# Performance work log

Measured on AMD Instinct MI355X. Metric: run time of the kernel, lower is better.

Reference implementation:

```python
import jax, jax.numpy as jnp
import numpy as np

HEADS, POINTS = 8, 4
EPS = 1e-5
BS, C, H, W = 2, 256, 200, 200


def _layernorm(x, g, b):
    m = x.mean(-1, keepdims=True)
    v = ((x - m) ** 2).mean(-1, keepdims=True)
    return (x - m) / jnp.sqrt(v + EPS) * g + b


def _sine_pos(bs, Hh, Ww, num_feats, temperature=10000.0):
    # mmdet SinePositionalEncoding with all-zeros mask: cumsum of ones -> 1..H / 1..W
    y = jnp.arange(1, Hh + 1, dtype=jnp.float32)
    x = jnp.arange(1, Ww + 1, dtype=jnp.float32)
    dim_t = jnp.arange(num_feats, dtype=jnp.float32)
    dim_t = temperature ** (2.0 * jnp.floor(dim_t / 2.0) / num_feats)

    def interleave(p):  # p: [N, num_feats] -> [sin(p0),cos(p1),sin(p2),...]
        return jnp.stack((jnp.sin(p[:, 0::2]), jnp.cos(p[:, 1::2])), axis=-1).reshape(p.shape[0], -1)

    pos_x = interleave(x[:, None] / dim_t)  # [W, nf]
    pos_y = interleave(y[:, None] / dim_t)  # [H, nf]
    pos = jnp.concatenate([
        jnp.broadcast_to(pos_y[:, None, :], (Hh, Ww, num_feats)),
        jnp.broadcast_to(pos_x[None, :, :], (Hh, Ww, num_feats)),
    ], axis=-1)  # [H, W, 2*nf] (channel order matches cat((pos_y,pos_x),dim=1) after flatten/permute)
    return jnp.broadcast_to(pos.reshape(1, Hh * Ww, 2 * num_feats), (bs, Hh * Ww, 2 * num_feats))


def _bilinear_sample(v, x, y):
    # v: [bs, heads, H, W, hd]; x, y: [bs, heads, N] pixel coords (align_corners=False, zero padding)
    bs, nh, Hh, Ww, hd = v.shape
    vf = v.reshape(bs, nh, Hh * Ww, hd)
    x0 = jnp.floor(x)
    y0 = jnp.floor(y)
    wx = x - x0
    wy = y - y0

    def gather(xi, yi):
        valid = (xi >= 0) & (xi < Ww) & (yi >= 0) & (yi < Hh)
        xc = jnp.clip(xi, 0, Ww - 1).astype(jnp.int32)
        yc = jnp.clip(yi, 0, Hh - 1).astype(jnp.int32)
        idx = yc * Ww + xc
        g = jnp.take_along_axis(vf, idx[..., None], axis=2)  # [bs, nh, N, hd]
        return g * valid[..., None].astype(v.dtype)

    out = gather(x0, y0) * ((1 - wx) * (1 - wy))[..., None]
    out = out + gather(x0 + 1, y0) * (wx * (1 - wy))[..., None]
    out = out + gather(x0, y0 + 1) * ((1 - wx) * wy)[..., None]
    out = out + gather(x0 + 1, y0 + 1) * (wx * wy)[..., None]
    return out


def _dfa_layer(out, ref, pos, Hh, Ww, p):
    bs, Lq, Cc = out.shape
    hd = Cc // HEADS
    q = out + pos
    value = out @ p['vp_w'].T + p['vp_b']  # [bs, Lq, C]
    off = (q @ p['off_w'].T + p['off_b']).reshape(bs, Lq, HEADS, POINTS, 2)
    aw = jax.nn.softmax((q @ p['aw_w'].T + p['aw_b']).reshape(bs, Lq, HEADS, POINTS), axis=-1)
    norm = jnp.array([Ww, Hh], dtype=out.dtype)
    loc = ref[None, :, None, None, :] + off / norm  # [bs, Lq, heads, P, 2] normalized [0,1]
    x = loc[..., 0] * Ww - 0.5
    y = loc[..., 1] * Hh - 0.5
    v = value.reshape(bs, Lq, HEADS, hd).transpose(0, 2, 1, 3).reshape(bs, HEADS, Hh, Ww, hd)
    xt = x.transpose(0, 2, 1, 3).reshape(bs, HEADS, Lq * POINTS)
    yt = y.transpose(0, 2, 1, 3).reshape(bs, HEADS, Lq * POINTS)
    samp = _bilinear_sample(v, xt, yt).reshape(bs, HEADS, Lq, POINTS, hd)
    attn = jnp.einsum('bhqpd,bqhp->bqhd', samp, aw).reshape(bs, Lq, Cc)
    attn = attn @ p['op_w'].T + p['op_b']
    out = _layernorm(out + attn, p['ln1_g'], p['ln1_b'])
    ffn = jax.nn.relu(out @ p['l1_w'].T + p['l1_b']) @ p['l2_w'].T + p['l2_b']
    return _layernorm(out + ffn, p['ln2_g'], p['ln2_b'])


def setup_inputs() -> dict:
    key = jax.random.key(0)
    ks = jax.random.split(key, 20)
    s = 0.02
    L = 3
    return {
        'bev_feat': jax.random.normal(ks[0], (BS, C, H, W), jnp.float32),
        'proj_q_w': jax.random.normal(ks[1], (C, C), jnp.float32) * s,
        'proj_q_b': jax.random.normal(ks[2], (C,), jnp.float32) * s,
        'off_w': jax.random.normal(ks[3], (L, HEADS * POINTS * 2, C), jnp.float32) * s,
        'off_b': jax.random.normal(ks[4], (L, HEADS * POINTS * 2), jnp.float32) * s,
        'aw_w': jax.random.normal(ks[5], (L, HEADS * POINTS, C), jnp.float32) * s,
        'aw_b': jax.random.normal(ks[6], (L, HEADS * POINTS), jnp.float32) * s,
        'vp_w': jax.random.normal(ks[7], (L, C, C), jnp.float32) * s,
        'vp_b': jax.random.normal(ks[8], (L, C), jnp.float32) * s,
        'op_w': jax.random.normal(ks[9], (L, C, C), jnp.float32) * s,
        'op_b': jax.random.normal(ks[10], (L, C), jnp.float32) * s,
        'ln1_g': jnp.ones((L, C), jnp.float32),
        'ln1_b': jnp.zeros((L, C), jnp.float32),
        'l1_w': jax.random.normal(ks[11], (L, C, C), jnp.float32) * s,
        'l1_b': jax.random.normal(ks[12], (L, C), jnp.float32) * s,
        'l2_w': jax.random.normal(ks[13], (L, C, C), jnp.float32) * s,
        'l2_b': jax.random.normal(ks[14], (L, C), jnp.float32) * s,
        'ln2_g': jnp.ones((L, C), jnp.float32),
        'ln2_b': jnp.zeros((L, C), jnp.float32),
    }


def reference(bev_feat, proj_q_w, proj_q_b, off_w, off_b, aw_w, aw_b, vp_w, vp_b,
              op_w, op_b, ln1_g, ln1_b, l1_w, l1_b, l2_w, l2_b, ln2_g, ln2_b):
    bs, Cc, Hh, Ww = bev_feat.shape
    x = bev_feat.reshape(bs, Cc, Hh * Ww).transpose(0, 2, 1)  # [bs, HW, C]
    out = x @ proj_q_w.T + proj_q_b
    # reference points: pixel centers normalized to [0,1]
    ry, rx = jnp.meshgrid(jnp.linspace(0.5, Hh - 0.5, Hh) / Hh,
                          jnp.linspace(0.5, Ww - 0.5, Ww) / Ww, indexing='ij')
    ref = jnp.stack([rx.reshape(-1), ry.reshape(-1)], axis=-1).astype(bev_feat.dtype)  # [HW, 2]
    pos = _sine_pos(bs, Hh, Ww, Cc // 2).astype(bev_feat.dtype)
    n_layers = off_w.shape[0]
    for i in range(n_layers):
        p = dict(off_w=off_w[i], off_b=off_b[i], aw_w=aw_w[i], aw_b=aw_b[i],
                 vp_w=vp_w[i], vp_b=vp_b[i], op_w=op_w[i], op_b=op_b[i],
                 ln1_g=ln1_g[i], ln1_b=ln1_b[i], l1_w=l1_w[i], l1_b=l1_b[i],
                 l2_w=l2_w[i], l2_b=l2_b[i], ln2_g=ln2_g[i], ln2_b=ln2_b[i])
        out = _dfa_layer(out, ref, pos, Hh, Ww, p)
    return out.transpose(0, 2, 1).reshape(bs, Cc, Hh, Ww)
```

## Files before the change

### kernel.cpp

```cpp
#include <hip/hip_runtime.h>
#include <math.h>

#define HEADS 8
#define POINTS 4
#define BSZ 2
#define CDIM 256
#define HH 200
#define WW 200
#define LQ (HH * WW)
#define MTOT (BSZ * LQ)
#define NLAYERS 3

typedef __attribute__((ext_vector_type(8))) short shortx8;
typedef __attribute__((ext_vector_type(4))) float floatx4;

__device__ __forceinline__ ushort f2b(float f) {
    union { float f; unsigned u; } v; v.f = f;
    unsigned r = v.u + 0x7fffu + ((v.u >> 16) & 1u);
    return (ushort)(r >> 16);
}
__device__ __forceinline__ float b2f(ushort b) {
    union { unsigned u; float f; } v; v.u = ((unsigned)b) << 16;
    return v.f;
}
__device__ __forceinline__ float bitsf(unsigned u) {
    union { unsigned u; float f; } v; v.u = u;
    return v.f;
}
__device__ __forceinline__ uint packbf(float lo, float hi) {
    return (uint)f2b(lo) | ((uint)f2b(hi) << 16);
}

__global__ __launch_bounds__(256)
void cvt_kernel(const float* __restrict__ in, ushort* __restrict__ out)
{
    const int i = (blockIdx.x * 256 + threadIdx.x) * 4;
    const float4 v = *(const float4*)(in + i);
    ushort4 o;
    o.x = f2b(v.x); o.y = f2b(v.y); o.z = f2b(v.z); o.w = f2b(v.w);
    *(ushort4*)(out + i) = o;
}

__global__ __launch_bounds__(256)
void build_offaw(const float* __restrict__ offw, const float* __restrict__ offb,
                 const float* __restrict__ aww, const float* __restrict__ awb,
                 ushort* __restrict__ wout, float* __restrict__ bout)
{
    const int blk = blockIdx.x;
    const int i = blk >> 7;
    const int r = blk & 127;
    const int c = threadIdx.x;
    float v = 0.f;
    if (r < 64)      v = offw[((size_t)i * 64 + r) * CDIM + c];
    else if (r < 96) v = aww[((size_t)i * 32 + (r - 64)) * CDIM + c];
    wout[((size_t)i * 128 + r) * CDIM + c] = f2b(v);
    if (c == 0) {
        float bb = 0.f;
        if (r < 64)      bb = offb[i * 64 + r];
        else if (r < 96) bb = awb[i * 32 + (r - 64)];
        bout[i * 128 + r] = bb;
    }
}

__global__ __launch_bounds__(256)
void pos_kernel(ushort* __restrict__ pos)
{
    const int idx = blockIdx.x * 256 + threadIdx.x;
    const int c = idx & 255;
    const int l = idx >> 8;
    const int cc = c & 127;
    const float coord = (c < 128) ? (float)(l / WW + 1) : (float)(l % WW + 1);
    const float expo = (float)(2 * (cc >> 1)) * (1.0f / 128.0f);
    const float t = powf(10000.0f, expo);
    const float ph = coord / t;
    pos[idx] = f2b((cc & 1) ? cosf(ph) : sinf(ph));
}

__global__ __launch_bounds__(256)
void bevT_kernel(const float* __restrict__ in, ushort* __restrict__ out)
{
    __shared__ float tile[32][33];
    const int b = blockIdx.z;
    const int l0 = blockIdx.x * 32;
    const int c0 = blockIdx.y * 32;
    const float* ib = in + (size_t)b * CDIM * LQ;
    ushort* ob = out + (size_t)b * LQ * CDIM;
    #pragma unroll
    for (int j = 0; j < 32; j += 8)
        tile[threadIdx.y + j][threadIdx.x] =
            ib[(size_t)(c0 + threadIdx.y + j) * LQ + l0 + threadIdx.x];
    __syncthreads();
    #pragma unroll
    for (int j = 0; j < 32; j += 8)
        ob[(size_t)(l0 + threadIdx.y + j) * CDIM + c0 + threadIdx.x] =
            f2b(tile[threadIdx.x][threadIdx.y + j]);
}

#define LSTR 40

template<bool RELU, bool F32OUT, bool BF16OUT, bool QOUT>
__global__ __launch_bounds__(256)
void mfma_gemm(const ushort* __restrict__ A, const ushort* __restrict__ B,
               const float* __restrict__ bias,
               float* __restrict__ Cf, ushort* __restrict__ Cb,
               ushort* __restrict__ Cq, const ushort* __restrict__ posb,
               int N, int K)
{
    __shared__ ushort As[128 * LSTR];
    __shared__ ushort Bs[128 * LSTR];
    const int tid = threadIdx.x;
    const int lane = tid & 63;
    const int wave = tid >> 6;
    const int wr = (wave >> 1) * 64;
    const int wc = (wave & 1) * 64;
    const int rowBase = blockIdx.y * 128;
    const int colBase = blockIdx.x * 128;

    floatx4 acc[4][4];
    #pragma unroll
    for (int i = 0; i < 4; i++)
        #pragma unroll
        for (int j = 0; j < 4; j++) {
            floatx4 z = {0.f, 0.f, 0.f, 0.f};
            acc[i][j] = z;
        }

    const int strow = tid >> 2;
    const int stcol = (tid & 3) * 8;
    const int kq = (lane >> 4) * 8;
    const int lr = lane & 15;

    for (int k0 = 0; k0 < K; k0 += 32) {
        #pragma unroll
        for (int j = 0; j < 2; j++) {
            const int r = j * 64 + strow;
            const uint4 av = *(const uint4*)(A + (size_t)(rowBase + r) * K + k0 + stcol);
            const uint4 bv = *(const uint4*)(B + (size_t)(colBase + r) * K + k0 + stcol);
            *(uint4*)(As + r * LSTR + stcol) = av;
            *(uint4*)(Bs + r * LSTR + stcol) = bv;
        }
        __syncthreads();
        shortx8 af[4], bfr[4];
        #pragma unroll
        for (int t = 0; t < 4; t++) {
            af[t]  = *(const shortx8*)(As + (wr + t * 16 + lr) * LSTR + kq);
            bfr[t] = *(const shortx8*)(Bs + (wc + t * 16 + lr) * LSTR + kq);
        }
        #pragma unroll
        for (int mt = 0; mt < 4; mt++)
            #pragma unroll
            for (int nt = 0; nt < 4; nt++)
                acc[mt][nt] = __builtin_amdgcn_mfma_f32_16x16x32_bf16(
                    af[mt], bfr[nt], acc[mt][nt], 0, 0, 0);
        __syncthreads();
    }

    const int colB = colBase + wc + lr;
    const int rowB = rowBase + wr + (lane >> 4) * 4;
    #pragma unroll
    for (int mt = 0; mt < 4; mt++) {
        #pragma unroll
        for (int r = 0; r < 4; r++) {
            const int m = rowB + mt * 16 + r;
            const int pr = (m >= LQ) ? m - LQ : m;
            #pragma unroll
            for (int nt = 0; nt < 4; nt++) {
                const int n = colB + nt * 16;
                float v = acc[mt][nt][r] + bias[n];
                if (RELU) v = fmaxf(v, 0.f);
                if (F32OUT) Cf[(size_t)m * N + n] = v;
                if (BF16OUT) Cb[(size_t)m * N + n] = f2b(v);
                if (QOUT) {
                    const float pv = b2f(posb[(size_t)pr * CDIM + n]);
                    Cq[(size_t)m * N + n] = f2b(v + pv);
                }
            }
        }
    }
}

template<bool RELU, bool LN, bool F32OUT, bool BF16OUT, bool QOUT, bool PERMW>
__global__ __launch_bounds__(256)
void gemm_fused(const ushort* __restrict__ A, const ushort* __restrict__ B,
                const float* __restrict__ bias,
                float* __restrict__ resid, ushort* __restrict__ Cb,
                ushort* __restrict__ Cq, const ushort* __restrict__ posb,
                const float* __restrict__ g, const float* __restrict__ beta)
{
    __shared__ ushort As[64 * LSTR];
    __shared__ ushort Bs[256 * LSTR];
    __shared__ float2 red[64][4];

    const int tid = threadIdx.x;
    const int lane = tid & 63;
    const int wave = tid >> 6;
    const int lr = lane & 15;
    const int hi = lane >> 4;
    const int rowBase = blockIdx.x * 64;
    const int wc = wave * 64;

    floatx4 acc[4][4];
    #pragma unroll
    for (int i = 0; i < 4; i++)
        #pragma unroll
        for (int j = 0; j < 4; j++) {
            floatx4 z = {0.f, 0.f, 0.f, 0.f};
            acc[i][j] = z;
        }

    const int strow = tid >> 2;
    const int stcol = (tid & 3) * 8;
    const int kq = hi * 8;

    const ushort* ag = A + (size_t)(rowBase + strow) * CDIM + stcol;
    const ushort* bg = B + (size_t)strow * CDIM + stcol;

    for (int k0 = 0; k0 < CDIM; k0 += 32) {
        const uint4 av  = *(const uint4*)(ag + k0);
        const uint4 bv0 = *(const uint4*)(bg + k0);
        const uint4 bv1 = *(const uint4*)(bg + k0 + 64 * CDIM);
        const uint4 bv2 = *(const uint4*)(bg + k0 + 128 * CDIM);
        const uint4 bv3 = *(const uint4*)(bg + k0 + 192 * CDIM);
        *(uint4*)(As + strow * LSTR + stcol) = av;
        *(uint4*)(Bs + strow * LSTR + stcol) = bv0;
        *(uint4*)(Bs + (strow + 64) * LSTR + stcol) = bv1;
        *(uint4*)(Bs + (strow + 128) * LSTR + stcol) = bv2;
        *(uint4*)(Bs + (strow + 192) * LSTR + stcol) = bv3;
        __syncthreads();
        shortx8 af[4], bfr[4];
        #pragma unroll
        for (int t = 0; t < 4; t++) {
            af[t]  = *(const shortx8*)(As + (t * 16 + lr) * LSTR + kq);
            bfr[t] = *(const shortx8*)(Bs + (wc + t * 16 + lr) * LSTR + kq);
        }
        #pragma unroll
        for (int mt = 0; mt < 4; mt++)
            #pragma unroll
            for (int nt = 0; nt < 4; nt++)
                acc[mt][nt] = __builtin_amdgcn_mfma_f32_16x16x32_bf16(
                    af[mt], bfr[nt], acc[mt][nt], 0, 0, 0);
        __syncthreads();
    }

    float bcol[4];
    #pragma unroll
    for (int nt = 0; nt < 4; nt++) bcol[nt] = bias[wc + nt * 16 + lr];

    float* pbase = resid + (size_t)blockIdx.x * (64 * CDIM) + wave * 4096 + lane * 64;

    if (LN) {
        #pragma unroll
        for (int mt = 0; mt < 4; mt++) {
            float4 rv[4];
            #pragma unroll
            for (int r = 0; r < 4; r++)
                rv[r] = *(const float4*)(pbase + mt * 16 + r * 4);
            #pragma unroll
            for (int r = 0; r < 4; r++) {
                const int mrel = mt * 16 + hi * 4 + r;
                float s = 0.f, sq = 0.f;
                #pragma unroll
                for (int nt = 0; nt < 4; nt++) {
                    float x = acc[mt][nt][r] + bcol[nt] + (&rv[r].x)[nt];
                    acc[mt][nt][r] = x;
                    s += x; sq += x * x;
                }
                #pragma unroll
                for (int o = 8; o >= 1; o >>= 1) {
                    s  += __shfl_xor(s, o, 64);
                    sq += __shfl_xor(sq, o, 64);
                }
                if (lr == 0) { float2 t2; t2.x = s; t2.y = sq; red[mrel][wave] = t2; }
            }
        }
        __syncthreads();
        float gcol[4], btcol[4];
        #pragma unroll
        for (int nt = 0; nt < 4; nt++) {
            gcol[nt]  = g[wc + nt * 16 + lr];
            btcol[nt] = beta[wc + nt * 16 + lr];
        }
        #pragma unroll
        for (int mt = 0; mt < 4; mt++) {
            #pragma unroll
            for (int r = 0; r < 4; r++) {
                const int mrel = mt * 16 + hi * 4 + r;
                const int m = rowBase + mrel;
                const float2 t0 = red[mrel][0], t1 = red[mrel][1];
                const float2 t2 = red[mrel][2], t3 = red[mrel][3];
                const float S  = (t0.x + t1.x) + (t2.x + t3.x);
                const float SQ = (t0.y + t1.y) + (t2.y + t3.y);
                const float mean = S * (1.0f / CDIM);
                const float var = SQ * (1.0f / CDIM) - mean * mean;
                const float rstd = rsqrtf(var + 1e-5f);
                const int pr = (m >= LQ) ? m - LQ : m;
                float4 wv;
                #pragma unroll
                for (int nt = 0; nt < 4; nt++) {
                    const int col = wc + nt * 16 + lr;
                    const float y = (acc[mt][nt][r] - mean) * rstd * gcol[nt] + btcol[nt];
                    if (PERMW) (&wv.x)[nt] = y;
                    else       resid[(size_t)m * CDIM + col] = y;
                    if (BF16OUT) Cb[(size_t)m * CDIM + col] = f2b(y);
                    if (QOUT) Cq[(size_t)m * CDIM + col] =
                        f2b(y + b2f(posb[(size_t)pr * CDIM + col]));
                }
                if (PERMW) *(float4*)(pbase + mt * 16 + r * 4) = wv;
            }
        }
    } else {
        #pragma unroll
        for (int mt = 0; mt < 4; mt++) {
            #pragma unroll
            for (int r = 0; r < 4; r++) {
                const int m = rowBase + mt * 16 + hi * 4 + r;
                const int pr = (m >= LQ) ? m - LQ : m;
                float4 wv;
                #pragma unroll
                for (int nt = 0; nt < 4; nt++) {
                    const int col = wc + nt * 16 + lr;
                    float y = acc[mt][nt][r] + bcol[nt];
                    if (RELU) y = fmaxf(y, 0.f);
                    if (F32OUT) {
                        if (PERMW) (&wv.x)[nt] = y;
                        else       resid[(size_t)m * CDIM + col] = y;
                    }
                    if (BF16OUT) Cb[(size_t)m * CDIM + col] = f2b(y);
                    if (QOUT) Cq[(size_t)m * CDIM + col] =
                        f2b(y + b2f(posb[(size_t)pr * CDIM + col]));
                }
                if (F32OUT && PERMW) *(float4*)(pbase + mt * 16 + r * 4) = wv;
            }
        }
    }
}

__global__ __launch_bounds__(256)
void sample_kernel(const ushort* __restrict__ val,
                   const float* __restrict__ offaw,
                   ushort* __restrict__ attn)
{
    const int tid = threadIdx.x;
    const int m = blockIdx.x * 8 + (tid >> 5);
    const int lane = tid & 31;
    const int head = lane >> 2;
    const int c = head * 32 + (lane & 3) * 8;
    const int b = (m >= LQ) ? 1 : 0;
    const int l = m - (b ? LQ : 0);

    const float* row = offaw + (size_t)m * 128;
    const float4 lg  = *(const float4*)(row + 64 + head * 4);
    const float4 o01 = *(const float4*)(row + head * 8);
    const float4 o23 = *(const float4*)(row + head * 8 + 4);

    const float mx = fmaxf(fmaxf(lg.x, lg.y), fmaxf(lg.z, lg.w));
    const float e0 = expf(lg.x - mx), e1 = expf(lg.y - mx);
    const float e2 = expf(lg.z - mx), e3 = expf(lg.w - mx);
    const float inv = 1.0f / (e0 + e1 + e2 + e3);
    const float awv[4] = {e0 * inv, e1 * inv, e2 * inv, e3 * inv};

    const float lx = (float)(l % WW);
    const float ly = (float)(l / WW);
    const float px[4] = {lx + o01.x, lx + o01.z, lx + o23.x, lx + o23.z};
    const float py[4] = {ly + o01.y, ly + o01.w, ly + o23.y, ly + o23.w};

    const ushort* vb = val + (size_t)b * LQ * CDIM;
    uint4 cv[16];
    float cw[16];
    #pragma unroll
    for (int p = 0; p < POINTS; p++) {
        const float x = px[p], y = py[p];
        const float xf = floorf(x), yf = floorf(y);
        const int x0 = (int)xf, y0 = (int)yf;
        const float wx = x - xf, wy = y - yf;
        const int x0c = min(max(x0, 0), WW - 1);
        const int x1c = min(max(x0 + 1, 0), WW - 1);
        const int y0c = min(max(y0, 0), HH - 1);
        const int y1c = min(max(y0 + 1, 0), HH - 1);
        const float vx0 = (x0 >= 0 && x0 < WW) ? 1.f : 0.f;
        const float vx1 = (x0 + 1 >= 0 && x0 + 1 < WW) ? 1.f : 0.f;
        const float vy0 = (y0 >= 0 && y0 < HH) ? 1.f : 0.f;
        const float vy1 = (y0 + 1 >= 0 && y0 + 1 < HH) ? 1.f : 0.f;
        const float a = awv[p];
        cw[p * 4 + 0] = a * (1.f - wx) * (1.f - wy) * vx0 * vy0;
        cw[p * 4 + 1] = a * wx * (1.f - wy) * vx1 * vy0;
        cw[p * 4 + 2] = a * (1.f - wx) * wy * vx0 * vy1;
        cw[p * 4 + 3] = a * wx * wy * vx1 * vy1;
        const int r0 = y0c * WW, r1 = y1c * WW;
        cv[p * 4 + 0] = *(const uint4*)(vb + (((unsigned)(r0 + x0c)) << 8) + c);
        cv[p * 4 + 1] = *(const uint4*)(vb + (((unsigned)(r0 + x1c)) << 8) + c);
        cv[p * 4 + 2] = *(const uint4*)(vb + (((unsigned)(r1 + x0c)) << 8) + c);
        cv[p * 4 + 3] = *(const uint4*)(vb + (((unsigned)(r1 + x1c)) << 8) + c);
    }
    float a0 = 0.f, a1 = 0.f, a2 = 0.f, a3 = 0.f;
    float a4 = 0.f, a5 = 0.f, a6 = 0.f, a7 = 0.f;
    #pragma unroll
    for (int i = 0; i < 16; i++) {
        const float wgt = cw[i];
        a0 = fmaf(wgt, bitsf(cv[i].x << 16), a0);
        a1 = fmaf(wgt, bitsf(cv[i].x & 0xffff0000u), a1);
        a2 = fmaf(wgt, bitsf(cv[i].y << 16), a2);
        a3 = fmaf(wgt, bitsf(cv[i].y & 0xffff0000u), a3);
        a4 = fmaf(wgt, bitsf(cv[i].z << 16), a4);
        a5 = fmaf(wgt, bitsf(cv[i].z & 0xffff0000u), a5);
        a6 = fmaf(wgt, bitsf(cv[i].w << 16), a6);
        a7 = fmaf(wgt, bitsf(cv[i].w & 0xffff0000u), a7);
    }
    uint4 o;
    o.x = packbf(a0, a1); o.y = packbf(a2, a3);
    o.z = packbf(a4, a5); o.w = packbf(a6, a7);
    *(uint4*)(attn + (size_t)m * CDIM + c) = o;
}

__global__ __launch_bounds__(256)
void transpose_out(const float* __restrict__ in, float* __restrict__ outp)
{
    __shared__ float tile[32][33];
    const int b = blockIdx.z;
    const int l0 = blockIdx.x * 32;
    const int c0 = blockIdx.y * 32;
    const float* ib = in + (size_t)b * LQ * CDIM;
    float* ob = outp + (size_t)b * CDIM * LQ;
    #pragma unroll
    for (int j = 0; j < 32; j += 8)
        tile[threadIdx.y + j][threadIdx.x] =
            ib[(size_t)(l0 + threadIdx.y + j) * CDIM + c0 + threadIdx.x];
    __syncthreads();
    #pragma unroll
    for (int j = 0; j < 32; j += 8)
        ob[(size_t)(c0 + threadIdx.y + j) * LQ + l0 + threadIdx.x] =
            tile[threadIdx.x][threadIdx.y + j];
}

extern "C" void kernel_launch(void* const* d_in, const int* in_sizes, int n_in,
                              void* d_out, int out_size, void* d_ws, size_t ws_size,
                              hipStream_t stream)
{
    const float* bev      = (const float*)d_in[0];
    const float* proj_q_w = (const float*)d_in[1];
    const float* proj_q_b = (const float*)d_in[2];
    const float* off_w    = (const float*)d_in[3];
    const float* off_b    = (const float*)d_in[4];
    const float* aw_w     = (const float*)d_in[5];
    const float* aw_b     = (const float*)d_in[6];
    const float* vp_w     = (const float*)d_in[7];
    const float* vp_b     = (const float*)d_in[8];
    const float* op_w     = (const float*)d_in[9];
    const float* op_b     = (const float*)d_in[10];
    const float* ln1_g    = (const float*)d_in[11];
    const float* ln1_b    = (const float*)d_in[12];
    const float* l1_w     = (const float*)d_in[13];
    const float* l1_b     = (const float*)d_in[14];
    const float* l2_w     = (const float*)d_in[15];
    const float* l2_b     = (const float*)d_in[16];
    const float* ln2_g    = (const float*)d_in[17];
    const float* ln2_b    = (const float*)d_in[18];
    float* outp = (float*)d_out;

    char* w = (char*)d_ws;
    float*  out_f   = (float*)(w);
    float*  offaw_f = (float*)(w + 81920000);
    ushort* out_b   = (ushort*)(w + 163840000);
    ushort* q_b     = (ushort*)(w + 204800000);
    ushort* val_b   = (ushort*)(w + 245760000);
    ushort* pos_b   = (ushort*)(w + 286720000);
    ushort* w_b     = (ushort*)(w + 307200000);
    ushort* wproj = w_b;
    ushort* wvp   = w_b + 65536;
    ushort* wop   = w_b + 65536 + 196608;
    ushort* wl1   = w_b + 65536 + 2 * 196608;
    ushort* wl2   = w_b + 65536 + 3 * 196608;
    ushort* wofa  = w_b + 65536 + 4 * 196608;
    float*  bofa  = (float*)(w + 307200000 + 2 * (65536 + 4 * 196608 + 98304));

    const dim3 blk(256);

    cvt_kernel<<<dim3(65536 / 1024), blk, 0, stream>>>(proj_q_w, wproj);
    cvt_kernel<<<dim3(196608 / 1024), blk, 0, stream>>>(vp_w, wvp);
    cvt_kernel<<<dim3(196608 / 1024), blk, 0, stream>>>(op_w, wop);
    cvt_kernel<<<dim3(196608 / 1024), blk, 0, stream>>>(l1_w, wl1);
    cvt_kernel<<<dim3(196608 / 1024), blk, 0, stream>>>(l2_w, wl2);
    build_offaw<<<dim3(3 * 128), blk, 0, stream>>>(off_w, off_b, aw_w, aw_b, wofa, bofa);
    pos_kernel<<<dim3((LQ * CDIM) / 256), blk, 0, stream>>>(pos_b);
    bevT_kernel<<<dim3(LQ / 32, CDIM / 32, BSZ), dim3(32, 8), 0, stream>>>(bev, val_b);

    const dim3 gF(MTOT / 64);
    const dim3 g128(1, MTOT / 128);

    gemm_fused<false, false, true, true, true, true><<<gF, blk, 0, stream>>>(
        val_b, wproj, proj_q_b, out_f, out_b, q_b, pos_b, nullptr, nullptr);

    for (int i = 0; i < NLAYERS; i++) {
        gemm_fused<false, false, false, true, false, false><<<gF, blk, 0, stream>>>(
            out_b, wvp + (size_t)i * 65536, vp_b + (size_t)i * CDIM,
            nullptr, val_b, nullptr, nullptr, nullptr, nullptr);
        mfma_gemm<false, true, false, false><<<g128, blk, 0, stream>>>(
            q_b, wofa + (size_t)i * 32768, bofa + (size_t)i * 128,
            offaw_f, nullptr, nullptr, nullptr, 128, CDIM);
        sample_kernel<<<dim3(MTOT / 8), blk, 0, stream>>>(val_b, offaw_f, q_b);
        gemm_fused<false, true, false, true, false, true><<<gF, blk, 0, stream>>>(
            q_b, wop + (size_t)i * 65536, op_b + (size_t)i * CDIM,
            out_f, out_b, nullptr, pos_b,
            ln1_g + (size_t)i * CDIM, ln1_b + (size_t)i * CDIM);
        gemm_fused<true, false, false, true, false, false><<<gF, blk, 0, stream>>>(
            out_b, wl1 + (size_t)i * 65536, l1_b + (size_t)i * CDIM,
            nullptr, val_b, nullptr, nullptr, nullptr, nullptr);
        if (i < NLAYERS - 1) {
            gemm_fused<false, true, false, true, true, true><<<gF, blk, 0, stream>>>(
                val_b, wl2 + (size_t)i * 65536, l2_b + (size_t)i * CDIM,
                out_f, out_b, q_b, pos_b,
                ln2_g + (size_t)i * CDIM, ln2_b + (size_t)i * CDIM);
        } else {
            gemm_fused<false, true, false, false, false, false><<<gF, blk, 0, stream>>>(
                val_b, wl2 + (size_t)i * 65536, l2_b + (size_t)i * CDIM,
                out_f, nullptr, nullptr, pos_b,
                ln2_g + (size_t)i * CDIM, ln2_b + (size_t)i * CDIM);
        }
    }

    transpose_out<<<dim3(LQ / 32, CDIM / 32, BSZ), dim3(32, 8), 0, stream>>>(out_f, outp);
}
```

Before: 1.124 ms.

## Permute channel layout so fused GEMM epilogues write vectorized row stores

Introduces a fixed channel permutation within 64-column groups and applies it consistently to weights (vp, l1, l2, off/aw), positional encodings and the final transpose. With it, each lane's four output columns become contiguous, so GEMM epilogues emit float4/ushort4 stores for the residual, bf16 and query outputs instead of scattered scalar stores. The old per-lane 'PERMW' scratch layout for the fp32 residual is replaced by normal row-major addressing, and the LayerNorm reduction buffer now reuses the As shared memory. The risk is correctness: every producer and consumer of the permuted layout must agree, including the sampling kernel and the un-permute in the output transpose.

```diff
diff --git a/kernel.cpp b/kernel.cpp
--- a/kernel.cpp
+++ b/kernel.cpp
@@ -31,6 +31,13 @@
     return (uint)f2b(lo) | ((uint)f2b(hi) << 16);
 }
 
+__device__ __forceinline__ int permc(int c) {
+    return (c & ~63) | (((c & 15) << 2) | ((c & 63) >> 4));
+}
+__device__ __forceinline__ int iperm(int p) {
+    return (p & ~63) | (((p & 3) << 4) | ((p & 63) >> 2));
+}
+
 __global__ __launch_bounds__(256)
 void cvt_kernel(const float* __restrict__ in, ushort* __restrict__ out)
 {
@@ -39,6 +46,20 @@
     ushort4 o;
     o.x = f2b(v.x); o.y = f2b(v.y); o.z = f2b(v.z); o.w = f2b(v.w);
     *(ushort4*)(out + i) = o;
+}
+
+__global__ __launch_bounds__(256)
+void cvt_perm_kernel(const float* __restrict__ in, ushort* __restrict__ out)
+{
+    const int idx = (blockIdx.x * 256 + threadIdx.x) * 4;
+    const int rowb = idx & ~255;
+    const int p0 = idx & 255;
+    ushort4 o;
+    o.x = f2b(in[rowb + iperm(p0 + 0)]);
+    o.y = f2b(in[rowb + iperm(p0 + 1)]);
+    o.z = f2b(in[rowb + iperm(p0 + 2)]);
+    o.w = f2b(in[rowb + iperm(p0 + 3)]);
+    *(ushort4*)(out + idx) = o;
 }
 
 __global__ __launch_bounds__(256)
@@ -53,7 +74,7 @@
     float v = 0.f;
     if (r < 64)      v = offw[((size_t)i * 64 + r) * CDIM + c];
     else if (r < 96) v = aww[((size_t)i * 32 + (r - 64)) * CDIM + c];
-    wout[((size_t)i * 128 + r) * CDIM + c] = f2b(v);
+    wout[((size_t)i * 128 + r) * CDIM + permc(c)] = f2b(v);
     if (c == 0) {
         float bb = 0.f;
         if (r < 64)      bb = offb[i * 64 + r];
@@ -73,7 +94,7 @@
     const float expo = (float)(2 * (cc >> 1)) * (1.0f / 128.0f);
     const float t = powf(10000.0f, expo);
     const float ph = coord / t;
-    pos[idx] = f2b((cc & 1) ? cosf(ph) : sinf(ph));
+    pos[(size_t)l * CDIM + permc(c)] = f2b((cc & 1) ? cosf(ph) : sinf(ph));
 }
 
 __global__ __launch_bounds__(256)
@@ -179,7 +200,7 @@
     }
 }
 
-template<bool RELU, bool LN, bool F32OUT, bool BF16OUT, bool QOUT, bool PERMW>
+template<bool RELU, bool LN, bool F32OUT, bool BF16OUT, bool QOUT, bool PERMC>
 __global__ __launch_bounds__(256)
 void gemm_fused(const ushort* __restrict__ A, const ushort* __restrict__ B,
                 const float* __restrict__ bias,
@@ -189,7 +210,6 @@
 {
     __shared__ ushort As[64 * LSTR];
     __shared__ ushort Bs[256 * LSTR];
-    __shared__ float2 red[64][4];
 
     const int tid = threadIdx.x;
     const int lane = tid & 63;
@@ -246,22 +266,19 @@
     #pragma unroll
     for (int nt = 0; nt < 4; nt++) bcol[nt] = bias[wc + nt * 16 + lr];
 
-    float* pbase = resid + (size_t)blockIdx.x * (64 * CDIM) + wave * 4096 + lane * 64;
-
     if (LN) {
+        float2 (*red)[4] = (float2(*)[4])As;
         #pragma unroll
         for (int mt = 0; mt < 4; mt++) {
-            float4 rv[4];
-            #pragma unroll
-            for (int r = 0; r < 4; r++)
-                rv[r] = *(const float4*)(pbase + mt * 16 + r * 4);
             #pragma unroll
             for (int r = 0; r < 4; r++) {
                 const int mrel = mt * 16 + hi * 4 + r;
+                const int m = rowBase + mrel;
+                const float4 rv = *(const float4*)(resid + (size_t)m * CDIM + wc + lr * 4);
                 float s = 0.f, sq = 0.f;
                 #pragma unroll
                 for (int nt = 0; nt < 4; nt++) {
-                    float x = acc[mt][nt][r] + bcol[nt] + (&rv[r].x)[nt];
+                    float x = acc[mt][nt][r] + bcol[nt] + (&rv.x)[nt];
                     acc[mt][nt][r] = x;
                     s += x; sq += x * x;
                 }
@@ -295,17 +312,19 @@
                 const float rstd = rsqrtf(var + 1e-5f);
                 const int pr = (m >= LQ) ? m - LQ : m;
                 float4 wv;
+                ushort4 ob, qq;
+                ushort4 pp;
+                if (QOUT) pp = *(const ushort4*)(posb + (size_t)pr * CDIM + wc + lr * 4);
                 #pragma unroll
                 for (int nt = 0; nt < 4; nt++) {
-                    const int col = wc + nt * 16 + lr;
                     const float y = (acc[mt][nt][r] - mean) * rstd * gcol[nt] + btcol[nt];
-                    if (PERMW) (&wv.x)[nt] = y;
-                    else       resid[(size_t)m * CDIM + col] = y;
-                    if (BF16OUT) Cb[(size_t)m * CDIM + col] = f2b(y);
-                    if (QOUT) Cq[(size_t)m * CDIM + col] =
-                        f2b(y + b2f(posb[(size_t)pr * CDIM + col]));
+                    (&wv.x)[nt] = y;
+                    if (BF16OUT) (&ob.x)[nt] = f2b(y);
+                    if (QOUT)    (&qq.x)[nt] = f2b(y + b2f((&pp.x)[nt]));
                 }
-                if (PERMW) *(float4*)(pbase + mt * 16 + r * 4) = wv;
+                *(float4*)(resid + (size_t)m * CDIM + wc + lr * 4) = wv;
+                if (BF16OUT) *(ushort4*)(Cb + (size_t)m * CDIM + wc + lr * 4) = ob;
+                if (QOUT)    *(ushort4*)(Cq + (size_t)m * CDIM + wc + lr * 4) = qq;
             }
         }
     } else {
@@ -316,20 +335,29 @@
                 const int m = rowBase + mt * 16 + hi * 4 + r;
                 const int pr = (m >= LQ) ? m - LQ : m;
                 float4 wv;
+                ushort4 ob, qq, pp;
+                if (QOUT && PERMC)
+                    pp = *(const ushort4*)(posb + (size_t)pr * CDIM + wc + lr * 4);
                 #pragma unroll
                 for (int nt = 0; nt < 4; nt++) {
-                    const int col = wc + nt * 16 + lr;
                     float y = acc[mt][nt][r] + bcol[nt];
                     if (RELU) y = fmaxf(y, 0.f);
-                    if (F32OUT) {
-                        if (PERMW) (&wv.x)[nt] = y;
-                        else       resid[(size_t)m * CDIM + col] = y;
+                    (&wv.x)[nt] = y;
+                    if (PERMC) {
+                        if (BF16OUT) (&ob.x)[nt] = f2b(y);
+                        if (QOUT)    (&qq.x)[nt] = f2b(y + b2f((&pp.x)[nt]));
+                    } else {
+                        const int col = wc + nt * 16 + lr;
+                        if (BF16OUT) Cb[(size_t)m * CDIM + col] = f2b(y);
+                        if (QOUT) Cq[(size_t)m * CDIM + col] =
+                            f2b(y + b2f(posb[(size_t)pr * CDIM + col]));
                     }
-                    if (BF16OUT) Cb[(size_t)m * CDIM + col] = f2b(y);
-                    if (QOUT) Cq[(size_t)m * CDIM + col] =
-                        f2b(y + b2f(posb[(size_t)pr * CDIM + col]));
                 }
-                if (F32OUT && PERMW) *(float4*)(pbase + mt * 16 + r * 4) = wv;
+                if (F32OUT) *(float4*)(resid + (size_t)m * CDIM + wc + lr * 4) = wv;
+                if (PERMC && BF16OUT)
+                    *(ushort4*)(Cb + (size_t)m * CDIM + wc + lr * 4) = ob;
+                if (PERMC && QOUT)
+                    *(ushort4*)(Cq + (size_t)m * CDIM + wc + lr * 4) = qq;
             }
         }
     }
@@ -428,7 +456,7 @@
     __syncthreads();
     #pragma unroll
     for (int j = 0; j < 32; j += 8)
-        ob[(size_t)(c0 + threadIdx.y + j) * LQ + l0 + threadIdx.x] =
+        ob[(size_t)iperm(c0 + threadIdx.y + j) * LQ + l0 + threadIdx.x] =
             tile[threadIdx.x][threadIdx.y + j];
 }
 
@@ -476,10 +504,10 @@
     const dim3 blk(256);
 
     cvt_kernel<<<dim3(65536 / 1024), blk, 0, stream>>>(proj_q_w, wproj);
-    cvt_kernel<<<dim3(196608 / 1024), blk, 0, stream>>>(vp_w, wvp);
+    cvt_perm_kernel<<<dim3(196608 / 1024), blk, 0, stream>>>(vp_w, wvp);
     cvt_kernel<<<dim3(196608 / 1024), blk, 0, stream>>>(op_w, wop);
-    cvt_kernel<<<dim3(196608 / 1024), blk, 0, stream>>>(l1_w, wl1);
-    cvt_kernel<<<dim3(196608 / 1024), blk, 0, stream>>>(l2_w, wl2);
+    cvt_perm_kernel<<<dim3(196608 / 1024), blk, 0, stream>>>(l1_w, wl1);
+    cvt_perm_kernel<<<dim3(196608 / 1024), blk, 0, stream>>>(l2_w, wl2);
     build_offaw<<<dim3(3 * 128), blk, 0, stream>>>(off_w, off_b, aw_w, aw_b, wofa, bofa);
     pos_kernel<<<dim3((LQ * CDIM) / 256), blk, 0, stream>>>(pos_b);
     bevT_kernel<<<dim3(LQ / 32, CDIM / 32, BSZ), dim3(32, 8), 0, stream>>>(bev, val_b);
@@ -502,7 +530,7 @@
             q_b, wop + (size_t)i * 65536, op_b + (size_t)i * CDIM,
             out_f, out_b, nullptr, pos_b,
             ln1_g + (size_t)i * CDIM, ln1_b + (size_t)i * CDIM);
-        gemm_fused<true, false, false, true, false, false><<<gF, blk, 0, stream>>>(
+        gemm_fused<true, false, false, true, false, true><<<gF, blk, 0, stream>>>(
             out_b, wl1 + (size_t)i * 65536, l1_b + (size_t)i * CDIM,
             nullptr, val_b, nullptr, nullptr, nullptr, nullptr);
         if (i < NLAYERS - 1) {
@@ -511,7 +539,7 @@
                 out_f, out_b, q_b, pos_b,
                 ln2_g + (size_t)i * CDIM, ln2_b + (size_t)i * CDIM);
         } else {
-            gemm_fused<false, true, false, false, false, false><<<gF, blk, 0, stream>>>(
+            gemm_fused<false, true, false, false, false, true><<<gF, blk, 0, stream>>>(
                 val_b, wl2 + (size_t)i * 65536, l2_b + (size_t)i * CDIM,
                 out_f, nullptr, nullptr, pos_b,
                 ln2_g + (size_t)i * CDIM, ln2_b + (size_t)i * CDIM);
```

After: 1.026 ms. 1.1x faster.
